# Performance work log

Measured on AMD Instinct MI355X. Metric: run time of the kernel, lower is better.

The kernel has to match this reference:

```python
import jax, jax.numpy as jnp
import numpy as np

A1, A2, X0, D, CUTOFF = 0.06, 1.005, 0.145, 0.033, 2.0

def photonic_sigmoid(x):
    # x[x - x0 > cutoff] clamped at cutoff, then logistic-like response
    z = jnp.minimum(x - X0, CUTOFF)
    return A2 + (A1 - A2) / (1.0 + jnp.exp(z / D))

def setup_inputs() -> dict:
    key = jax.random.key(0)
    k1, k2, k3 = jax.random.split(key, 3)
    T, B, I, H = 256, 4096, 144, 32
    x = jax.random.normal(k1, (T, B, I), dtype=jnp.float32)
    # fc1.weight: [H, H+I] (torch layout out x in), fc1.bias: [H]
    W = jax.random.normal(k2, (H, H + I), dtype=jnp.float32) * (1.0 / np.sqrt(H + I))
    b = jax.random.normal(k3, (H,), dtype=jnp.float32) * 0.01
    return {"x": x, "W": W, "b": b}

def reference(x, W, b):
    T, B, I = x.shape
    H = W.shape[0]
    # concat([h, x_t]) @ W.T == h @ Wh.T + x_t @ Wx.T (split avoids per-step concat)
    Wh = W[:, :H]   # [H, H]
    Wx = W[:, H:]   # [H, I]
    h0 = jnp.zeros((B, H), dtype=x.dtype)

    def step(h, xt):
        z = h @ Wh.T + xt @ Wx.T + b  # [B, H]
        h_new = photonic_sigmoid(z)
        return h_new, None

    h_final, _ = jax.lax.scan(step, h0, x)
    return h_final
```

## Files before the change

kernel.cpp:

```cpp
#include <hip/hip_runtime.h>

#define T_STEPS 256
#define B_SZ    4096
#define I_SZ    144
#define H_SZ    32
#define W_LD    176

#define PS_A1   0.06f
#define PS_A2   1.005f
#define PS_X0   0.145f
#define PS_D    0.033f
#define PS_CUT  2.0f

typedef const __attribute__((address_space(1))) float* gas_fp;
typedef __attribute__((address_space(3))) float* las_fp;

__device__ __forceinline__ void dma16(const float* g, float* l) {
    __builtin_amdgcn_global_load_lds((gas_fp)g, (las_fp)l, 16, 0, 0);
}

__device__ __forceinline__ float psig(float z) {
    const float expC = (float)(1.0 / (0.033 * 0.6931471805599453));
    float zz = fminf(z - PS_X0, PS_CUT);
    float e  = exp2f(zz * expC);
#if __has_builtin(__builtin_amdgcn_rcpf)
    float r = __builtin_amdgcn_rcpf(1.0f + e);
#else
    float r = 1.0f / (1.0f + e);
#endif
    return fmaf(PS_A1 - PS_A2, r, PS_A2);
}

__global__ __launch_bounds__(64, 4) void fused_rnn(
    const float* __restrict__ x,
    const float* __restrict__ W,
    const float* __restrict__ bias,
    float* __restrict__ out)
{
    const int tid = threadIdx.x;
    const int j   = tid & 15;
    const int q   = tid >> 4;
    const int b   = blockIdx.x;

    __shared__ float vbuf[4][256];

    float wA[44], wB[44];
    {
        const float* wa = W + j * W_LD + q * 44;
        const float* wb = W + (j + 16) * W_LD + q * 44;
#pragma unroll
        for (int i = 0; i < 11; ++i) {
            float4 va = *(const float4*)(wa + 4 * i);
            float4 vc = *(const float4*)(wb + 4 * i);
            wA[4*i+0] = va.x; wA[4*i+1] = va.y; wA[4*i+2] = va.z; wA[4*i+3] = va.w;
            wB[4*i+0] = vc.x; wB[4*i+1] = vc.y; wB[4*i+2] = vc.z; wB[4*i+3] = vc.w;
        }
    }
    const float biasA = bias[j];
    const float biasB = bias[j + 16];

    asm volatile("s_waitcnt vmcnt(0)" ::: "memory");

    if (q == 0) { vbuf[0][j] = 0.0f; vbuf[0][16 + j] = 0.0f; }

    const size_t tstride = (size_t)B_SZ * I_SZ;
    const float* xrow = x + (size_t)b * I_SZ + tid * 4;
    const bool ld = (tid < 36);

    if (ld) {
        dma16(xrow,           &vbuf[0][H_SZ]);
        dma16(xrow + tstride, &vbuf[1][H_SZ]);
    }
    const float* xsrc = xrow + 2 * tstride;

    float h0 = 0.0f, h1 = 0.0f;

    for (int t = 0; t < T_STEPS; ++t) {
        if (ld) dma16(xsrc, &vbuf[(t + 2) & 3][H_SZ]);
        if (t < T_STEPS - 3) xsrc += tstride;

        asm volatile("s_waitcnt vmcnt(2)" ::: "memory");
        __builtin_amdgcn_sched_barrier(0);

        const float* vb = &vbuf[t & 3][q * 44];
        float a0=0.f, a1=0.f, a2=0.f, a3=0.f;
        float c0=0.f, c1=0.f, c2=0.f, c3=0.f;
#pragma unroll
        for (int i = 0; i < 11; ++i) {
            float4 v = *(const float4*)(vb + 4 * i);
            a0 = fmaf(wA[4*i+0], v.x, a0);
            a1 = fmaf(wA[4*i+1], v.y, a1);
            a2 = fmaf(wA[4*i+2], v.z, a2);
            a3 = fmaf(wA[4*i+3], v.w, a3);
            c0 = fmaf(wB[4*i+0], v.x, c0);
            c1 = fmaf(wB[4*i+1], v.y, c1);
            c2 = fmaf(wB[4*i+2], v.z, c2);
            c3 = fmaf(wB[4*i+3], v.w, c3);
        }
        float pA = (a0 + a1) + (a2 + a3);
        float pB = (c0 + c1) + (c2 + c3);
        pA += __shfl_xor(pA, 16, 64);
        pA += __shfl_xor(pA, 32, 64);
        pB += __shfl_xor(pB, 16, 64);
        pB += __shfl_xor(pB, 32, 64);

        h0 = psig(pA + biasA);
        h1 = psig(pB + biasB);

        if (q == 0) {
            vbuf[(t + 1) & 3][j]      = h0;
            vbuf[(t + 1) & 3][16 + j] = h1;
        }
    }

    if (q == 0) {
        out[b * H_SZ + j]      = h0;
        out[b * H_SZ + 16 + j] = h1;
    }
}

extern "C" void kernel_launch(void* const* d_in, const int* in_sizes, int n_in,
                              void* d_out, int out_size, void* d_ws, size_t ws_size,
                              hipStream_t stream)
{
    const float* x    = (const float*)d_in[0];
    const float* W    = (const float*)d_in[1];
    const float* bias = (const float*)d_in[2];
    float* out = (float*)d_out;
    (void)d_ws; (void)ws_size; (void)in_sizes; (void)n_in; (void)out_size;

    fused_rnn<<<B_SZ, 64, 0, stream>>>(x, W, bias, out);
}
```

Baseline: 889.0 us.

## Repartition RNN matvec across 8 K-slices with packed FMA and butterfly reduction

Each lane now owns 4 output rows and a 24-wide K slice, with 8 K-slices instead of 4. Partial sums are combined through a transpose-style butterfly of shuffles, so each lane ends up with one output instead of two. The inner loop uses v_pk_fma_f32 to issue two FMAs per instruction, which halves the FMA instruction count per recurrent step. The trade is a longer serial shuffle chain, select overhead, padding of the shared buffer to 192 entries with zeroed tail columns, and launch bounds relaxed from 4 to 3 waves.

New measurement: 913.2 us. 2.7% more time.

```diff
diff --git a/kernel.cpp b/kernel.cpp
--- a/kernel.cpp
+++ b/kernel.cpp
@@ -5,6 +5,7 @@
 #define I_SZ    144
 #define H_SZ    32
 #define W_LD    176
+#define VPAD    192
 
 #define PS_A1   0.06f
 #define PS_A2   1.005f
@@ -19,6 +20,12 @@
     __builtin_amdgcn_global_load_lds((gas_fp)g, (las_fp)l, 16, 0, 0);
 }
 
+__device__ __forceinline__ float2 pkfma(float2 a, float2 b, float2 c) {
+    float2 d;
+    asm("v_pk_fma_f32 %0, %1, %2, %3" : "=v"(d) : "v"(a), "v"(b), "v"(c));
+    return d;
+}
+
 __device__ __forceinline__ float psig(float z) {
     const float expC = (float)(1.0 / (0.033 * 0.6931471805599453));
     float zz = fminf(z - PS_X0, PS_CUT);
@@ -31,37 +38,42 @@
     return fmaf(PS_A1 - PS_A2, r, PS_A2);
 }
 
-__global__ __launch_bounds__(64, 4) void fused_rnn(
+__global__ __launch_bounds__(64, 3) void fused_rnn(
     const float* __restrict__ x,
     const float* __restrict__ W,
     const float* __restrict__ bias,
     float* __restrict__ out)
 {
     const int tid = threadIdx.x;
-    const int j   = tid & 15;
-    const int q   = tid >> 4;
+    const int j   = tid & 7;
+    const int s   = tid >> 3;
     const int b   = blockIdx.x;
 
-    __shared__ float vbuf[4][256];
+    __shared__ float vbuf[4][VPAD];
 
-    float wA[44], wB[44];
-    {
-        const float* wa = W + j * W_LD + q * 44;
-        const float* wb = W + (j + 16) * W_LD + q * 44;
+    float2 wp[4][12];
 #pragma unroll
-        for (int i = 0; i < 11; ++i) {
-            float4 va = *(const float4*)(wa + 4 * i);
-            float4 vc = *(const float4*)(wb + 4 * i);
-            wA[4*i+0] = va.x; wA[4*i+1] = va.y; wA[4*i+2] = va.z; wA[4*i+3] = va.w;
-            wB[4*i+0] = vc.x; wB[4*i+1] = vc.y; wB[4*i+2] = vc.z; wB[4*i+3] = vc.w;
+    for (int r = 0; r < 4; ++r) {
+        const float* wr = W + (j + 8 * r) * W_LD;
+#pragma unroll
+        for (int i = 0; i < 6; ++i) {
+            int col = 24 * s + 4 * i;
+            float4 wv = (col < W_LD) ? *(const float4*)(wr + col)
+                                     : make_float4(0.f, 0.f, 0.f, 0.f);
+            wp[r][2*i]   = make_float2(wv.x, wv.y);
+            wp[r][2*i+1] = make_float2(wv.z, wv.w);
         }
     }
-    const float biasA = bias[j];
-    const float biasB = bias[j + 16];
+
+    const int bit3 = s & 1;
+    const int bit4 = (s >> 1) & 1;
+    const int outrow = j + 8 * (2 * bit3 + bit4);
+    const float bsr = bias[outrow];
 
     asm volatile("s_waitcnt vmcnt(0)" ::: "memory");
 
-    if (q == 0) { vbuf[0][j] = 0.0f; vbuf[0][16 + j] = 0.0f; }
+    if (tid < 32) vbuf[0][tid] = 0.0f;
+    vbuf[tid >> 4][176 + (tid & 15)] = 0.0f;
 
     const size_t tstride = (size_t)B_SZ * I_SZ;
     const float* xrow = x + (size_t)b * I_SZ + tid * 4;
@@ -73,7 +85,7 @@
     }
     const float* xsrc = xrow + 2 * tstride;
 
-    float h0 = 0.0f, h1 = 0.0f;
+    float h = 0.0f;
 
     for (int t = 0; t < T_STEPS; ++t) {
         if (ld) dma16(xsrc, &vbuf[(t + 2) & 3][H_SZ]);
@@ -82,41 +94,40 @@
         asm volatile("s_waitcnt vmcnt(2)" ::: "memory");
         __builtin_amdgcn_sched_barrier(0);
 
-        const float* vb = &vbuf[t & 3][q * 44];
-        float a0=0.f, a1=0.f, a2=0.f, a3=0.f;
-        float c0=0.f, c1=0.f, c2=0.f, c3=0.f;
+        const float* vb = &vbuf[t & 3][24 * s];
+        float2 a0 = make_float2(0.f, 0.f), a1 = a0, a2 = a0, a3 = a0;
 #pragma unroll
-        for (int i = 0; i < 11; ++i) {
+        for (int i = 0; i < 6; ++i) {
             float4 v = *(const float4*)(vb + 4 * i);
-            a0 = fmaf(wA[4*i+0], v.x, a0);
-            a1 = fmaf(wA[4*i+1], v.y, a1);
-            a2 = fmaf(wA[4*i+2], v.z, a2);
-            a3 = fmaf(wA[4*i+3], v.w, a3);
-            c0 = fmaf(wB[4*i+0], v.x, c0);
-            c1 = fmaf(wB[4*i+1], v.y, c1);
-            c2 = fmaf(wB[4*i+2], v.z, c2);
-            c3 = fmaf(wB[4*i+3], v.w, c3);
+            float2 vlo = make_float2(v.x, v.y);
+            float2 vhi = make_float2(v.z, v.w);
+            a0 = pkfma(wp[0][2*i], vlo, a0); a0 = pkfma(wp[0][2*i+1], vhi, a0);
+            a1 = pkfma(wp[1][2*i], vlo, a1); a1 = pkfma(wp[1][2*i+1], vhi, a1);
+            a2 = pkfma(wp[2][2*i], vlo, a2); a2 = pkfma(wp[2][2*i+1], vhi, a2);
+            a3 = pkfma(wp[3][2*i], vlo, a3); a3 = pkfma(wp[3][2*i+1], vhi, a3);
         }
-        float pA = (a0 + a1) + (a2 + a3);
-        float pB = (c0 + c1) + (c2 + c3);
-        pA += __shfl_xor(pA, 16, 64);
-        pA += __shfl_xor(pA, 32, 64);
-        pB += __shfl_xor(pB, 16, 64);
-        pB += __shfl_xor(pB, 32, 64);
+        float p0 = a0.x + a0.y, p1 = a1.x + a1.y;
+        float p2 = a2.x + a2.y, p3 = a3.x + a3.y;
 
-        h0 = psig(pA + biasA);
-        h1 = psig(pB + biasB);
+        float ua = bit3 ? p0 : p2;
+        float ub = bit3 ? p1 : p3;
+        float uas = __shfl_xor(ua, 8, 64);
+        float ubs = __shfl_xor(ub, 8, 64);
+        float q0 = (bit3 ? p2 : p0) + uas;
+        float q1 = (bit3 ? p3 : p1) + ubs;
 
-        if (q == 0) {
-            vbuf[(t + 1) & 3][j]      = h0;
-            vbuf[(t + 1) & 3][16 + j] = h1;
-        }
+        float w0 = bit4 ? q0 : q1;
+        float wsv = __shfl_xor(w0, 16, 64);
+        float z   = (bit4 ? q1 : q0) + wsv;
+
+        z += __shfl_xor(z, 32, 64);
+
+        h = psig(z + bsr);
+
+        if (s < 4) vbuf[(t + 1) & 3][outrow] = h;
     }
 
-    if (q == 0) {
-        out[b * H_SZ + j]      = h0;
-        out[b * H_SZ + 16 + j] = h1;
-    }
+    if (s < 4) out[(size_t)b * H_SZ + outrow] = h;
 }
 
 extern "C" void kernel_launch(void* const* d_in, const int* in_sizes, int n_in,
```
